# Performance work log

Measured on AMD Instinct MI355X. Metric: run time of the kernel, lower is better.

Reference implementation:

```python
import jax, jax.numpy as jnp
import numpy as np

N_NODES = 100000
N_EDGES = 500000
D = 128        # node feat dim == output dim
DT = 128       # time encoding dim
DE = 128       # edge feat dim
B = 300
K = 2
NN = 20
N_HEADS = 2
N_LAYERS = 2


def setup_inputs() -> dict:
    key = jax.random.key(0)
    ks = jax.random.split(key, 20)
    s = 0.05
    inp = {
        "node_features": jax.random.normal(ks[0], (N_NODES, D), jnp.float32) * s,
        "edge_features": jax.random.normal(ks[1], (N_EDGES, DE), jnp.float32) * s,
        "time_w": jax.random.normal(ks[2], (1, DT), jnp.float32),
        "time_b": jax.random.normal(ks[3], (DT,), jnp.float32),
        "Wq": jax.random.normal(ks[4], (N_LAYERS, D + DT, D), jnp.float32) * s,
        "Wk": jax.random.normal(ks[5], (N_LAYERS, D + DT + DE, D), jnp.float32) * s,
        "Wv": jax.random.normal(ks[6], (N_LAYERS, D + DT + DE, D), jnp.float32) * s,
        "Wo": jax.random.normal(ks[7], (N_LAYERS, D, D), jnp.float32) * s,
        "fc1": jax.random.normal(ks[8], (N_LAYERS, 2 * D, D), jnp.float32) * s,
        "fc2": jax.random.normal(ks[9], (N_LAYERS, D, D), jnp.float32) * s,
        "source_nodes": jax.random.randint(ks[10], (B,), 0, N_NODES),
        "timestamps": jax.random.uniform(ks[11], (B,), jnp.float32, 500.0, 1000.0),
        "neigh2": jax.random.randint(ks[12], (B, K, NN), 0, N_NODES),
        "eidx2": jax.random.randint(ks[13], (B, K, NN), 0, N_EDGES),
        "etimes2": jax.random.uniform(ks[14], (B, K, NN), jnp.float32, 0.0, 500.0),
        "neigh1": jax.random.randint(ks[15], (B * K * NN, K, NN), 0, N_NODES),
        "eidx1": jax.random.randint(ks[16], (B * K * NN, K, NN), 0, N_EDGES),
        "etimes1": jax.random.uniform(ks[17], (B * K * NN, K, NN), jnp.float32, 0.0, 500.0),
    }
    return inp


def reference(node_features, edge_features, time_w, time_b,
              Wq, Wk, Wv, Wo, fc1, fc2,
              source_nodes, timestamps,
              neigh2, eidx2, etimes2,
              neigh1, eidx1, etimes1):
    d = node_features.shape[1]
    dh = d // N_HEADS

    def time_enc(t):  # t: [...] -> [..., DT], TGAT-style cosine time encoding
        return jnp.cos(t[..., None] * time_w[0] + time_b)

    def hop_agg(layer, src_nodes, ts, neigh, eidx, etimes, neigh_emb):
        # neigh/eidx/etimes: [b, K, NN]; neigh_emb: [b, K, NN, d]
        b = src_nodes.shape[0]
        kn = K * NN
        src = node_features[src_nodes]                         # [b, d]
        src_t = time_enc(jnp.zeros((b,), ts.dtype))            # [b, DT]
        deltas = ts[:, None, None] - etimes                    # [b, K, NN]
        et = time_enc(deltas.reshape(b, kn))                   # [b, kn, DT]
        ef = edge_features[eidx].reshape(b, kn, -1)            # [b, kn, DE]
        ne = neigh_emb.reshape(b, kn, -1)                      # [b, kn, d]
        mask = neigh.reshape(b, kn) == 0                       # padded neighbors

        q = jnp.concatenate([src, src_t], axis=-1) @ Wq[layer]            # [b, d]
        kv_in = jnp.concatenate([ne, et, ef], axis=-1)                    # [b, kn, d+DT+DE]
        kk = kv_in @ Wk[layer]                                            # [b, kn, d]
        vv = kv_in @ Wv[layer]

        qh = q.reshape(b, N_HEADS, dh)
        kh = kk.reshape(b, kn, N_HEADS, dh)
        vh = vv.reshape(b, kn, N_HEADS, dh)
        scores = jnp.einsum('bhd,bnhd->bhn', qh, kh) / jnp.sqrt(jnp.float32(dh))
        scores = jnp.where(mask[:, None, :], jnp.float32(-1e9), scores)
        attn = jax.nn.softmax(scores, axis=-1)                            # [b, h, kn]
        out = jnp.einsum('bhn,bnhd->bhd', attn, vh).reshape(b, d) @ Wo[layer]
        merged = jnp.concatenate([out, src], axis=-1)                     # [b, 2d]
        return jax.nn.relu(merged @ fc1[layer]) @ fc2[layer]              # [b, d]

    # --- recursion unrolled (n_layers = 2) ---
    # level 0: raw node features of 2-hop neighbors
    b1 = neigh2.shape[0] * K * NN
    emb0 = node_features[neigh1.reshape(-1)].reshape(b1, K, NN, d)
    ts1 = jnp.repeat(timestamps, K * NN)
    # level 1 aggregation (attention_models[0])
    emb1 = hop_agg(0, neigh2.reshape(-1), ts1, neigh1, eidx1, etimes1, emb0)
    # level 2 aggregation (attention_models[1])
    emb2 = hop_agg(1, source_nodes, timestamps,
                   neigh2, eidx2, etimes2,
                   emb1.reshape(source_nodes.shape[0], K, NN, d))
    return emb2
```

## Files before the change

### kernel.cpp

```cpp
#include <hip/hip_runtime.h>

typedef _Float16 half_t;
typedef _Float16 half8  __attribute__((ext_vector_type(8)));
typedef _Float16 half4_t __attribute__((ext_vector_type(4)));
typedef float    floatx4 __attribute__((ext_vector_type(4)));

#define KNN 40

__global__ __launch_bounds__(256) void precompute_kernel(
    const float* __restrict__ Wq, const float* __restrict__ Wk,
    const float* __restrict__ Wv, const float* __restrict__ Wo,
    const float* __restrict__ fc1, const float* __restrict__ time_b,
    half_t* __restrict__ WkvT, float* __restrict__ qbias,
    float* __restrict__ Wofc1)
{
  int blk = blockIdx.x, tid = threadIdx.x;
  if (blk < 768) {
    int t = blk * 256 + tid;
    int l = t / 98304;
    int r = t - l * 98304;
    int n = r / 384;
    int k = r - n * 384;
    float v = (n < 128) ? Wk[l * 49152 + k * 128 + n]
                        : Wv[l * 49152 + k * 128 + (n - 128)];
    WkvT[t] = (half_t)v;
  } else if (blk == 768) {
    int l = tid >> 7, j = tid & 127;
    float s = 0.f;
    for (int d = 0; d < 128; ++d)
      s += cosf(time_b[d]) * Wq[l * 32768 + (128 + d) * 128 + j];
    qbias[l * 128 + j] = s;
  } else {
    int t = (blk - 769) * 256 + tid;
    int l = t >> 14;
    int r = t & 16383;
    int dd = r >> 7, j = r & 127;
    float s = 0.f;
    for (int m = 0; m < 128; ++m)
      s += Wo[l * 16384 + dd * 128 + m] * fc1[l * 32768 + m * 128 + j];
    Wofc1[t] = s;
  }
}

__global__ __launch_bounds__(256, 2) void hop_kernel(
    const float* __restrict__ nf,
    const float* __restrict__ ne_src,
    int ne_direct,
    const float* __restrict__ ef,
    const int*   __restrict__ src_idx,
    const float* __restrict__ tsv, int ts_div,
    const int*   __restrict__ neigh,
    const int*   __restrict__ eidx,
    const float* __restrict__ etimes,
    const float* __restrict__ tw,
    const float* __restrict__ tb,
    const float* __restrict__ Wq_l,
    const float* __restrict__ qbias_l,
    const half_t* __restrict__ WkvT_l,
    const float* __restrict__ Wofc1_l,
    const float* __restrict__ fc1b_l,
    const float* __restrict__ fc2_l,
    float* __restrict__ out)
{
  __shared__ __align__(16) char smem[65472];
  half_t* As  = (half_t*)(smem);
  half_t* BTs = (half_t*)(smem + 18432);
  half_t* kvT = (half_t*)(smem);
  float*  qs   = (float*)(smem + 61440);
  float*  srcs = (float*)(smem + 62976);
  float*  scs  = (float*)(smem + 64512);
  float*  attO = (float*)(smem + 61440);
  float*  h1s  = (float*)(smem + 61440);

  const int tid = threadIdx.x;
  const int bbase = blockIdx.x * 3;

  for (int i = tid; i < 384; i += 256) {
    int g = i >> 7, dd = i & 127;
    int sn = src_idx[bbase + g];
    srcs[i] = nf[(size_t)sn * 128 + dd];
  }
  __syncthreads();

  {
    int g = tid >> 7, jj = tid & 127;
    const float* sg = srcs + g * 128;
    float s = qbias_l[jj];
    for (int d = 0; d < 128; ++d) s += sg[d] * Wq_l[d * 128 + jj];
    qs[tid] = s;
    if (tid < 128) {
      const float* sg2 = srcs + 2 * 128;
      float s2 = qbias_l[jj];
      for (int d = 0; d < 128; ++d) s2 += sg2[d] * Wq_l[d * 128 + jj];
      qs[256 + tid] = s2;
    }
  }

  const int r = tid >> 1, hf = tid & 1;
  float dval = 0.f;
  const float* gbase_ne = nullptr;
  const float* gbase_ef = nullptr;
  if (r < 120) {
    int g = r / 40;
    int n = r - g * 40;
    int bg = bbase + g;
    int rowidx = bg * KNN + n;
    int nd = neigh[rowidx];
    int ed = eidx[rowidx];
    dval = tsv[bg / ts_div] - etimes[rowidx];
    gbase_ne = ne_direct ? (ne_src + (size_t)rowidx * 128)
                         : (ne_src + (size_t)nd * 128);
    gbase_ef = ef + (size_t)ed * 128;
  }

  floatx4 acc[4][8];
  #pragma unroll
  for (int mi = 0; mi < 4; ++mi)
    #pragma unroll
    for (int ni = 0; ni < 8; ++ni)
      acc[mi][ni] = (floatx4){0.f, 0.f, 0.f, 0.f};

  const int lane = tid & 63;
  const int wv   = tid >> 6;
  const int wm   = (wv & 1) * 64;
  const int wn   = (wv >> 1) * 128;
  const int l15  = lane & 15;
  const int q4   = lane >> 4;

  for (int kc = 0; kc < 6; ++kc) {
    const int seg  = kc >> 1;
    const int soff = (kc & 1) * 64;

    half_t* Arow = As + r * 72 + hf * 32;
    if (r < 120) {
      if (seg == 1) {
        #pragma unroll
        for (int i2 = 0; i2 < 4; ++i2) {
          half8 h;
          #pragma unroll
          for (int u = 0; u < 8; ++u) {
            int c = soff + hf * 32 + i2 * 8 + u;
            h[u] = (half_t)__cosf(__builtin_fmaf(dval, tw[c], tb[c]));
          }
          *(half8*)(Arow + i2 * 8) = h;
        }
      } else {
        const float* gb = (seg == 0 ? gbase_ne : gbase_ef) + soff + hf * 32;
        #pragma unroll
        for (int i2 = 0; i2 < 4; ++i2) {
          float4 v0 = ((const float4*)gb)[2 * i2];
          float4 v1 = ((const float4*)gb)[2 * i2 + 1];
          half8 h;
          h[0] = (half_t)v0.x; h[1] = (half_t)v0.y;
          h[2] = (half_t)v0.z; h[3] = (half_t)v0.w;
          h[4] = (half_t)v1.x; h[5] = (half_t)v1.y;
          h[6] = (half_t)v1.z; h[7] = (half_t)v1.w;
          *(half8*)(Arow + i2 * 8) = h;
        }
      }
    } else {
      half8 z = {};
      #pragma unroll
      for (int i2 = 0; i2 < 4; ++i2) *(half8*)(Arow + i2 * 8) = z;
    }

    {
      int p = tid & 3;
      #pragma unroll
      for (int j2 = 0; j2 < 4; ++j2) {
        int n2 = (tid >> 2) + j2 * 64;
        const uint4* gsrc = (const uint4*)(WkvT_l + (size_t)n2 * 384 + kc * 64 + p * 16);
        uint4 w0 = gsrc[0], w1 = gsrc[1];
        uint4* dst = (uint4*)(BTs + n2 * 72 + p * 16);
        dst[0] = w0; dst[1] = w1;
      }
    }
    __syncthreads();

    #pragma unroll
    for (int ks = 0; ks < 2; ++ks) {
      half8 a[4];
      #pragma unroll
      for (int mi = 0; mi < 4; ++mi)
        a[mi] = *(half8*)(As + (wm + mi * 16 + l15) * 72 + ks * 32 + q4 * 8);
      #pragma unroll
      for (int ni = 0; ni < 8; ++ni) {
        half8 b = *(half8*)(BTs + (wn + ni * 16 + l15) * 72 + ks * 32 + q4 * 8);
        #pragma unroll
        for (int mi = 0; mi < 4; ++mi)
          acc[mi][ni] = __builtin_amdgcn_mfma_f32_16x16x32_f16(a[mi], b, acc[mi][ni], 0, 0, 0);
      }
    }
    __syncthreads();
  }

  #pragma unroll
  for (int mi = 0; mi < 4; ++mi) {
    int m0 = wm + mi * 16 + q4 * 4;
    if (m0 < 120) {
      #pragma unroll
      for (int ni = 0; ni < 8; ++ni) {
        int col = wn + ni * 16 + l15;
        half4_t h;
        h[0] = (half_t)acc[mi][ni][0];
        h[1] = (half_t)acc[mi][ni][1];
        h[2] = (half_t)acc[mi][ni][2];
        h[3] = (half_t)acc[mi][ni][3];
        *(half4_t*)(kvT + col * 120 + m0) = h;
      }
    }
  }
  __syncthreads();

  if (tid < 240) {
    int g = tid / 80;
    int rem = tid - g * 80;
    int h = rem / 40;
    int n = rem - h * 40;
    int bg = bbase + g;
    bool masked = (neigh[bg * KNN + n] == 0);
    const float* qrow = qs + g * 128 + h * 64;
    int row = g * 40 + n;
    float s = 0.f;
    for (int d = 0; d < 64; ++d)
      s += qrow[d] * (float)kvT[(h * 64 + d) * 120 + row];
    scs[tid] = masked ? -1e9f : s * 0.125f;
  }
  __syncthreads();

  if (tid < 6) {
    float* sc = scs + tid * 40;
    float mx = -1e30f;
    for (int n = 0; n < 40; ++n) mx = fmaxf(mx, sc[n]);
    float sum = 0.f;
    for (int n = 0; n < 40; ++n) sum += __expf(sc[n] - mx);
    float inv = 1.f / sum;
    for (int n = 0; n < 40; ++n) sc[n] = __expf(sc[n] - mx) * inv;
  }
  __syncthreads();

  {
    float av0, av1 = 0.f;
    {
      int g = tid >> 7, dcol = tid & 127, h = dcol >> 6;
      const float* attn = scs + g * 80 + h * 40;
      const half_t* vcol = kvT + (128 + dcol) * 120 + g * 40;
      float s = 0.f;
      for (int n = 0; n < 40; ++n) s += attn[n] * (float)vcol[n];
      av0 = s;
    }
    if (tid < 128) {
      int dcol = tid, h = dcol >> 6;
      const float* attn = scs + 2 * 80 + h * 40;
      const half_t* vcol = kvT + (128 + dcol) * 120 + 2 * 40;
      float s = 0.f;
      for (int n = 0; n < 40; ++n) s += attn[n] * (float)vcol[n];
      av1 = s;
    }
    attO[tid] = av0;
    if (tid < 128) attO[256 + tid] = av1;
  }
  __syncthreads();

  float hv0, hv1 = 0.f;
  {
    int g = tid >> 7, jj = tid & 127;
    const float* ag = attO + g * 128;
    const float* sg = srcs + g * 128;
    float s = 0.f;
    for (int d = 0; d < 128; ++d)
      s += ag[d] * Wofc1_l[d * 128 + jj] + sg[d] * fc1b_l[d * 128 + jj];
    hv0 = fmaxf(s, 0.f);
  }
  if (tid < 128) {
    int jj = tid;
    const float* ag = attO + 2 * 128;
    const float* sg = srcs + 2 * 128;
    float s = 0.f;
    for (int d = 0; d < 128; ++d)
      s += ag[d] * Wofc1_l[d * 128 + jj] + sg[d] * fc1b_l[d * 128 + jj];
    hv1 = fmaxf(s, 0.f);
  }
  __syncthreads();
  h1s[tid] = hv0;
  if (tid < 128) h1s[256 + tid] = hv1;
  __syncthreads();

  {
    int g = tid >> 7, ii = tid & 127;
    const float* hg = h1s + g * 128;
    float s = 0.f;
    for (int j = 0; j < 128; ++j) s += hg[j] * fc2_l[j * 128 + ii];
    out[(size_t)(bbase + g) * 128 + ii] = s;
  }
  if (tid < 128) {
    int ii = tid;
    const float* hg = h1s + 2 * 128;
    float s = 0.f;
    for (int j = 0; j < 128; ++j) s += hg[j] * fc2_l[j * 128 + ii];
    out[(size_t)(bbase + 2) * 128 + ii] = s;
  }
}

extern "C" void kernel_launch(void* const* d_in, const int* in_sizes, int n_in,
                              void* d_out, int out_size, void* d_ws, size_t ws_size,
                              hipStream_t stream) {
  const float* nf      = (const float*)d_in[0];
  const float* ef      = (const float*)d_in[1];
  const float* tw      = (const float*)d_in[2];
  const float* tb      = (const float*)d_in[3];
  const float* Wq      = (const float*)d_in[4];
  const float* Wk      = (const float*)d_in[5];
  const float* Wv      = (const float*)d_in[6];
  const float* Wo      = (const float*)d_in[7];
  const float* fc1     = (const float*)d_in[8];
  const float* fc2     = (const float*)d_in[9];
  const int*   srcn    = (const int*)d_in[10];
  const float* ts      = (const float*)d_in[11];
  const int*   neigh2  = (const int*)d_in[12];
  const int*   eidx2   = (const int*)d_in[13];
  const float* etimes2 = (const float*)d_in[14];
  const int*   neigh1  = (const int*)d_in[15];
  const int*   eidx1   = (const int*)d_in[16];
  const float* etimes1 = (const float*)d_in[17];

  half_t* WkvT  = (half_t*)d_ws;
  float*  qbias = (float*)((char*)d_ws + 393216);
  float*  Wofc1 = (float*)((char*)d_ws + 394240);
  float*  emb1  = (float*)((char*)d_ws + 525312);

  precompute_kernel<<<dim3(897), dim3(256), 0, stream>>>(
      Wq, Wk, Wv, Wo, fc1, tb, WkvT, qbias, Wofc1);

  hop_kernel<<<dim3(4000), dim3(256), 0, stream>>>(
      nf, nf, 0, ef, neigh2, ts, 40, neigh1, eidx1, etimes1, tw, tb,
      Wq, qbias, WkvT, Wofc1, fc1 + 16384, fc2, emb1);

  hop_kernel<<<dim3(100), dim3(256), 0, stream>>>(
      nf, emb1, 1, ef, srcn, ts, 1, neigh2, eidx2, etimes2, tw, tb,
      Wq + 32768, qbias + 128, WkvT + 98304, Wofc1 + 16384,
      fc1 + 32768 + 16384, fc2 + 16384, (float*)d_out);
}
```

Before: 791.4 us.

## Use 512-thread blocks with swizzled MFMA LDS layout and smaller shared memory

Doubles the hop kernel's block size to 512 threads and halves the per-wave MFMA tile (acc 4x4 instead of 4x8), which lowers register pressure and allows more resident waves. The A/B shared-memory tiles move to a fragment-major layout without padding, and shared memory shrinks so more blocks fit per CU. The softmax becomes a wave-shuffle reduction and the V write-back is overlapped with it. The small tail matmuls run with one thread per output instead of doubling up. Risks: the K and V halves of kvT are now written in two phases into the same buffer, which is easy to get wrong, and the smaller per-wave tiles reuse each LDS load less.

```diff
diff --git a/kernel.cpp b/kernel.cpp
--- a/kernel.cpp
+++ b/kernel.cpp
@@ -6,6 +6,7 @@
 typedef float    floatx4 __attribute__((ext_vector_type(4)));
 
 #define KNN 40
+#define KVPAD 124
 
 __global__ __launch_bounds__(256) void precompute_kernel(
     const float* __restrict__ Wq, const float* __restrict__ Wk,
@@ -42,7 +43,7 @@
   }
 }
 
-__global__ __launch_bounds__(256, 2) void hop_kernel(
+__global__ __launch_bounds__(512, 4) void hop_kernel(
     const float* __restrict__ nf,
     const float* __restrict__ ne_src,
     int ne_direct,
@@ -62,130 +63,130 @@
     const float* __restrict__ fc2_l,
     float* __restrict__ out)
 {
-  __shared__ __align__(16) char smem[65472];
-  half_t* As  = (half_t*)(smem);
-  half_t* BTs = (half_t*)(smem + 18432);
-  half_t* kvT = (half_t*)(smem);
-  float*  qs   = (float*)(smem + 61440);
-  float*  srcs = (float*)(smem + 62976);
-  float*  scs  = (float*)(smem + 64512);
-  float*  attO = (float*)(smem + 61440);
-  float*  h1s  = (float*)(smem + 61440);
+  __shared__ __align__(16) char smem[53184];
+  half_t* As   = (half_t*)(smem);
+  half_t* BTs  = (half_t*)(smem + 16384);
+  half_t* kvT  = (half_t*)(smem + 16384);
+  float*  attO = (float*)(smem);
+  float*  h1s  = (float*)(smem + 1536);
+  float*  qs   = (float*)(smem + 49152);
+  float*  srcs = (float*)(smem + 50688);
+  float*  scs  = (float*)(smem + 52224);
 
   const int tid = threadIdx.x;
   const int bbase = blockIdx.x * 3;
 
-  for (int i = tid; i < 384; i += 256) {
-    int g = i >> 7, dd = i & 127;
-    int sn = src_idx[bbase + g];
-    srcs[i] = nf[(size_t)sn * 128 + dd];
-  }
-  __syncthreads();
-
-  {
+  if (tid < 384) {
+    int g = tid >> 7, dd = tid & 127;
+    srcs[tid] = nf[(size_t)src_idx[bbase + g] * 128 + dd];
+  }
+  __syncthreads();
+
+  if (tid < 384) {
     int g = tid >> 7, jj = tid & 127;
     const float* sg = srcs + g * 128;
     float s = qbias_l[jj];
+    #pragma unroll 8
     for (int d = 0; d < 128; ++d) s += sg[d] * Wq_l[d * 128 + jj];
     qs[tid] = s;
-    if (tid < 128) {
-      const float* sg2 = srcs + 2 * 128;
-      float s2 = qbias_l[jj];
-      for (int d = 0; d < 128; ++d) s2 += sg2[d] * Wq_l[d * 128 + jj];
-      qs[256 + tid] = s2;
-    }
-  }
-
-  const int r = tid >> 1, hf = tid & 1;
+  }
+
+  const int r = tid >> 2, p = tid & 3;
   float dval = 0.f;
-  const float* gbase_ne = nullptr;
-  const float* gbase_ef = nullptr;
+  const float* gb_ne = nullptr;
+  const float* gb_ef = nullptr;
   if (r < 120) {
     int g = r / 40;
     int n = r - g * 40;
     int bg = bbase + g;
     int rowidx = bg * KNN + n;
-    int nd = neigh[rowidx];
-    int ed = eidx[rowidx];
     dval = tsv[bg / ts_div] - etimes[rowidx];
-    gbase_ne = ne_direct ? (ne_src + (size_t)rowidx * 128)
-                         : (ne_src + (size_t)nd * 128);
-    gbase_ef = ef + (size_t)ed * 128;
-  }
-
-  floatx4 acc[4][8];
+    gb_ne = ne_direct ? (ne_src + (size_t)rowidx * 128)
+                      : (ne_src + (size_t)neigh[rowidx] * 128);
+    gb_ef = ef + (size_t)eidx[rowidx] * 128;
+  }
+
+  floatx4 acc[4][4];
   #pragma unroll
   for (int mi = 0; mi < 4; ++mi)
     #pragma unroll
-    for (int ni = 0; ni < 8; ++ni)
+    for (int ni = 0; ni < 4; ++ni)
       acc[mi][ni] = (floatx4){0.f, 0.f, 0.f, 0.f};
 
   const int lane = tid & 63;
   const int wv   = tid >> 6;
   const int wm   = (wv & 1) * 64;
-  const int wn   = (wv >> 1) * 128;
+  const int wn   = (wv >> 1) * 64;
   const int l15  = lane & 15;
   const int q4   = lane >> 4;
+
+  half_t* Adst = As + ((((r >> 4) * 8) + 2 * p) * 16 + (r & 15)) * 8;
+  const int bn = tid >> 1, pb = tid & 1;
+  half_t* Bdst = BTs + ((((bn >> 4) * 8) + pb * 4) * 16 + (bn & 15)) * 8;
 
   for (int kc = 0; kc < 6; ++kc) {
     const int seg  = kc >> 1;
     const int soff = (kc & 1) * 64;
 
-    half_t* Arow = As + r * 72 + hf * 32;
     if (r < 120) {
       if (seg == 1) {
-        #pragma unroll
-        for (int i2 = 0; i2 < 4; ++i2) {
-          half8 h;
-          #pragma unroll
-          for (int u = 0; u < 8; ++u) {
-            int c = soff + hf * 32 + i2 * 8 + u;
-            h[u] = (half_t)__cosf(__builtin_fmaf(dval, tw[c], tb[c]));
-          }
-          *(half8*)(Arow + i2 * 8) = h;
+        half8 h0, h1;
+        #pragma unroll
+        for (int u = 0; u < 8; ++u) {
+          int c = soff + p * 16 + u;
+          h0[u] = (half_t)__cosf(__builtin_fmaf(dval, tw[c], tb[c]));
         }
+        #pragma unroll
+        for (int u = 0; u < 8; ++u) {
+          int c = soff + p * 16 + 8 + u;
+          h1[u] = (half_t)__cosf(__builtin_fmaf(dval, tw[c], tb[c]));
+        }
+        *(half8*)(Adst)       = h0;
+        *(half8*)(Adst + 128) = h1;
       } else {
-        const float* gb = (seg == 0 ? gbase_ne : gbase_ef) + soff + hf * 32;
-        #pragma unroll
-        for (int i2 = 0; i2 < 4; ++i2) {
-          float4 v0 = ((const float4*)gb)[2 * i2];
-          float4 v1 = ((const float4*)gb)[2 * i2 + 1];
-          half8 h;
-          h[0] = (half_t)v0.x; h[1] = (half_t)v0.y;
-          h[2] = (half_t)v0.z; h[3] = (half_t)v0.w;
-          h[4] = (half_t)v1.x; h[5] = (half_t)v1.y;
-          h[6] = (half_t)v1.z; h[7] = (half_t)v1.w;
-          *(half8*)(Arow + i2 * 8) = h;
-        }
+        const float* gb = (seg == 0 ? gb_ne : gb_ef) + soff + p * 16;
+        float4 v0 = ((const float4*)gb)[0];
+        float4 v1 = ((const float4*)gb)[1];
+        float4 v2 = ((const float4*)gb)[2];
+        float4 v3 = ((const float4*)gb)[3];
+        half8 h0, h1;
+        h0[0] = (half_t)v0.x; h0[1] = (half_t)v0.y;
+        h0[2] = (half_t)v0.z; h0[3] = (half_t)v0.w;
+        h0[4] = (half_t)v1.x; h0[5] = (half_t)v1.y;
+        h0[6] = (half_t)v1.z; h0[7] = (half_t)v1.w;
+        h1[0] = (half_t)v2.x; h1[1] = (half_t)v2.y;
+        h1[2] = (half_t)v2.z; h1[3] = (half_t)v2.w;
+        h1[4] = (half_t)v3.x; h1[5] = (half_t)v3.y;
+        h1[6] = (half_t)v3.z; h1[7] = (half_t)v3.w;
+        *(half8*)(Adst)       = h0;
+        *(half8*)(Adst + 128) = h1;
       }
     } else {
       half8 z = {};
-      #pragma unroll
-      for (int i2 = 0; i2 < 4; ++i2) *(half8*)(Arow + i2 * 8) = z;
+      *(half8*)(Adst)       = z;
+      *(half8*)(Adst + 128) = z;
     }
 
     {
-      int p = tid & 3;
-      #pragma unroll
-      for (int j2 = 0; j2 < 4; ++j2) {
-        int n2 = (tid >> 2) + j2 * 64;
-        const uint4* gsrc = (const uint4*)(WkvT_l + (size_t)n2 * 384 + kc * 64 + p * 16);
-        uint4 w0 = gsrc[0], w1 = gsrc[1];
-        uint4* dst = (uint4*)(BTs + n2 * 72 + p * 16);
-        dst[0] = w0; dst[1] = w1;
-      }
+      const uint4* gsrc = (const uint4*)(WkvT_l + (size_t)bn * 384 + kc * 64 + pb * 32);
+      uint4 w0 = gsrc[0], w1 = gsrc[1], w2 = gsrc[2], w3 = gsrc[3];
+      *(uint4*)(Bdst)       = w0;
+      *(uint4*)(Bdst + 128) = w1;
+      *(uint4*)(Bdst + 256) = w2;
+      *(uint4*)(Bdst + 384) = w3;
     }
     __syncthreads();
 
     #pragma unroll
     for (int ks = 0; ks < 2; ++ks) {
+      const int c = ks * 4 + q4;
       half8 a[4];
       #pragma unroll
       for (int mi = 0; mi < 4; ++mi)
-        a[mi] = *(half8*)(As + (wm + mi * 16 + l15) * 72 + ks * 32 + q4 * 8);
+        a[mi] = *(half8*)(As + ((((wm >> 4) + mi) * 8 + c) * 16 + l15) * 8);
       #pragma unroll
-      for (int ni = 0; ni < 8; ++ni) {
-        half8 b = *(half8*)(BTs + (wn + ni * 16 + l15) * 72 + ks * 32 + q4 * 8);
+      for (int ni = 0; ni < 4; ++ni) {
+        half8 b = *(half8*)(BTs + ((((wn >> 4) + ni) * 8 + c) * 16 + l15) * 8);
         #pragma unroll
         for (int mi = 0; mi < 4; ++mi)
           acc[mi][ni] = __builtin_amdgcn_mfma_f32_16x16x32_f16(a[mi], b, acc[mi][ni], 0, 0, 0);
@@ -194,19 +195,21 @@
     __syncthreads();
   }
 
-  #pragma unroll
-  for (int mi = 0; mi < 4; ++mi) {
-    int m0 = wm + mi * 16 + q4 * 4;
-    if (m0 < 120) {
-      #pragma unroll
-      for (int ni = 0; ni < 8; ++ni) {
-        int col = wn + ni * 16 + l15;
-        half4_t h;
-        h[0] = (half_t)acc[mi][ni][0];
-        h[1] = (half_t)acc[mi][ni][1];
-        h[2] = (half_t)acc[mi][ni][2];
-        h[3] = (half_t)acc[mi][ni][3];
-        *(half4_t*)(kvT + col * 120 + m0) = h;
+  if (wv < 4) {
+    #pragma unroll
+    for (int mi = 0; mi < 4; ++mi) {
+      int row0 = wm + mi * 16 + q4 * 4;
+      if (row0 < 120) {
+        #pragma unroll
+        for (int ni = 0; ni < 4; ++ni) {
+          int col = wn + ni * 16 + l15;
+          half4_t h;
+          h[0] = (half_t)acc[mi][ni][0];
+          h[1] = (half_t)acc[mi][ni][1];
+          h[2] = (half_t)acc[mi][ni][2];
+          h[3] = (half_t)acc[mi][ni][3];
+          *(half4_t*)(kvT + col * KVPAD + row0) = h;
+        }
       }
     }
   }
@@ -217,88 +220,78 @@
     int rem = tid - g * 80;
     int h = rem / 40;
     int n = rem - h * 40;
-    int bg = bbase + g;
-    bool masked = (neigh[bg * KNN + n] == 0);
+    bool masked = (neigh[(bbase + g) * KNN + n] == 0);
     const float* qrow = qs + g * 128 + h * 64;
     int row = g * 40 + n;
     float s = 0.f;
+    #pragma unroll 8
     for (int d = 0; d < 64; ++d)
-      s += qrow[d] * (float)kvT[(h * 64 + d) * 120 + row];
+      s += qrow[d] * (float)kvT[(h * 64 + d) * KVPAD + row];
     scs[tid] = masked ? -1e9f : s * 0.125f;
   }
   __syncthreads();
 
-  if (tid < 6) {
-    float* sc = scs + tid * 40;
-    float mx = -1e30f;
-    for (int n = 0; n < 40; ++n) mx = fmaxf(mx, sc[n]);
-    float sum = 0.f;
-    for (int n = 0; n < 40; ++n) sum += __expf(sc[n] - mx);
-    float inv = 1.f / sum;
-    for (int n = 0; n < 40; ++n) sc[n] = __expf(sc[n] - mx) * inv;
-  }
-  __syncthreads();
-
-  {
-    float av0, av1 = 0.f;
-    {
-      int g = tid >> 7, dcol = tid & 127, h = dcol >> 6;
-      const float* attn = scs + g * 80 + h * 40;
-      const half_t* vcol = kvT + (128 + dcol) * 120 + g * 40;
-      float s = 0.f;
-      for (int n = 0; n < 40; ++n) s += attn[n] * (float)vcol[n];
-      av0 = s;
-    }
-    if (tid < 128) {
-      int dcol = tid, h = dcol >> 6;
-      const float* attn = scs + 2 * 80 + h * 40;
-      const half_t* vcol = kvT + (128 + dcol) * 120 + 2 * 40;
-      float s = 0.f;
-      for (int n = 0; n < 40; ++n) s += attn[n] * (float)vcol[n];
-      av1 = s;
-    }
-    attO[tid] = av0;
-    if (tid < 128) attO[256 + tid] = av1;
-  }
-  __syncthreads();
-
-  float hv0, hv1 = 0.f;
-  {
+  if (wv < 6) {
+    float v = (lane < 40) ? scs[wv * 40 + lane] : -1e30f;
+    float m = v;
+    #pragma unroll
+    for (int o = 32; o; o >>= 1) m = fmaxf(m, __shfl_xor(m, o));
+    float e = (lane < 40) ? __expf(v - m) : 0.f;
+    float ssum = e;
+    #pragma unroll
+    for (int o = 32; o; o >>= 1) ssum += __shfl_xor(ssum, o);
+    if (lane < 40) scs[wv * 40 + lane] = e / ssum;
+  }
+  if (wv >= 4) {
+    #pragma unroll
+    for (int mi = 0; mi < 4; ++mi) {
+      int row0 = wm + mi * 16 + q4 * 4;
+      if (row0 < 120) {
+        #pragma unroll
+        for (int ni = 0; ni < 4; ++ni) {
+          int col = wn - 128 + ni * 16 + l15;
+          half4_t h;
+          h[0] = (half_t)acc[mi][ni][0];
+          h[1] = (half_t)acc[mi][ni][1];
+          h[2] = (half_t)acc[mi][ni][2];
+          h[3] = (half_t)acc[mi][ni][3];
+          *(half4_t*)(kvT + col * KVPAD + row0) = h;
+        }
+      }
+    }
+  }
+  __syncthreads();
+
+  if (tid < 384) {
+    int g = tid >> 7, dcol = tid & 127, h = dcol >> 6;
+    const float* attn = scs + (g * 2 + h) * 40;
+    const half_t* vcol = kvT + dcol * KVPAD + g * 40;
+    float s = 0.f;
+    #pragma unroll 8
+    for (int n = 0; n < 40; ++n) s += attn[n] * (float)vcol[n];
+    attO[tid] = s;
+  }
+  __syncthreads();
+
+  if (tid < 384) {
     int g = tid >> 7, jj = tid & 127;
     const float* ag = attO + g * 128;
     const float* sg = srcs + g * 128;
     float s = 0.f;
+    #pragma unroll 8
     for (int d = 0; d < 128; ++d)
       s += ag[d] * Wofc1_l[d * 128 + jj] + sg[d] * fc1b_l[d * 128 + jj];
-    hv0 = fmaxf(s, 0.f);
-  }
-  if (tid < 128) {
-    int jj = tid;
-    const float* ag = attO + 2 * 128;
-    const float* sg = srcs + 2 * 128;
-    float s = 0.f;
-    for (int d = 0; d < 128; ++d)
-      s += ag[d] * Wofc1_l[d * 128 + jj] + sg[d] * fc1b_l[d * 128 + jj];
-    hv1 = fmaxf(s, 0.f);
-  }
-  __syncthreads();
-  h1s[tid] = hv0;
-  if (tid < 128) h1s[256 + tid] = hv1;
-  __syncthreads();
-
-  {
+    h1s[tid] = fmaxf(s, 0.f);
+  }
+  __syncthreads();
+
+  if (tid < 384) {
     int g = tid >> 7, ii = tid & 127;
     const float* hg = h1s + g * 128;
     float s = 0.f;
+    #pragma unroll 8
     for (int j = 0; j < 128; ++j) s += hg[j] * fc2_l[j * 128 + ii];
     out[(size_t)(bbase + g) * 128 + ii] = s;
-  }
-  if (tid < 128) {
-    int ii = tid;
-    const float* hg = h1s + 2 * 128;
-    float s = 0.f;
-    for (int j = 0; j < 128; ++j) s += hg[j] * fc2_l[j * 128 + ii];
-    out[(size_t)(bbase + 2) * 128 + ii] = s;
   }
 }
 
@@ -332,11 +325,11 @@
   precompute_kernel<<<dim3(897), dim3(256), 0, stream>>>(
       Wq, Wk, Wv, Wo, fc1, tb, WkvT, qbias, Wofc1);
 
-  hop_kernel<<<dim3(4000), dim3(256), 0, stream>>>(
+  hop_kernel<<<dim3(4000), dim3(512), 0, stream>>>(
       nf, nf, 0, ef, neigh2, ts, 40, neigh1, eidx1, etimes1, tw, tb,
       Wq, qbias, WkvT, Wofc1, fc1 + 16384, fc2, emb1);
 
-  hop_kernel<<<dim3(100), dim3(256), 0, stream>>>(
+  hop_kernel<<<dim3(100), dim3(512), 0, stream>>>(
       nf, emb1, 1, ef, srcn, ts, 1, neigh2, eidx2, etimes2, tw, tb,
       Wq + 32768, qbias + 128, WkvT + 98304, Wofc1 + 16384,
       fc1 + 32768 + 16384, fc2 + 16384, (float*)d_out);
```

After: 788.9 us. No clear change (-0.3%).
